# Performance work log

Measured on AMD Instinct MI355X. Metric: run time of the kernel, lower is better.

The kernel has to match this reference:

```python
import jax, jax.numpy as jnp
import numpy as np

B, S, D, H = 2, 2048, 1024, 16
HD = D // H  # 64

def setup_inputs() -> dict:
    key = jax.random.key(0)
    k1, k2, k3, k4, k5 = jax.random.split(key, 5)
    scale = 0.02
    return {
        "hidden_states": jax.random.normal(k1, (B, S, D), dtype=jnp.float32),
        "w_attn": jax.random.normal(k2, (D, 3 * D), dtype=jnp.float32) * scale,
        "b_attn": jax.random.normal(k3, (3 * D,), dtype=jnp.float32) * scale,
        "w_proj": jax.random.normal(k4, (D, D), dtype=jnp.float32) * scale,
        "b_proj": jax.random.normal(k5, (D,), dtype=jnp.float32) * scale,
    }

def reference(hidden_states, w_attn, b_attn, w_proj, b_proj):
    # qkv projection: [B,S,3D] -> split
    qkv = hidden_states @ w_attn + b_attn
    q, k, v = jnp.split(qkv, 3, axis=-1)
    # split heads -> [B,H,S,HD]
    def split_heads(t):
        return t.reshape(B, S, H, HD).transpose(0, 2, 1, 3)
    q, k, v = split_heads(q), split_heads(k), split_heads(v)
    # eager attention: full [B,H,S,S] scores, causal mask, softmax, AV
    scores = jnp.einsum('bhqd,bhkd->bhqk', q, k) / jnp.sqrt(jnp.float32(HD))
    causal = jnp.tril(jnp.ones((S, S), dtype=bool))  # [S,S]
    mask_value = jnp.finfo(scores.dtype).min
    scores = jnp.where(causal[None, None], scores, mask_value)
    attn = jax.nn.softmax(scores, axis=-1)
    out = jnp.einsum('bhqk,bhkd->bhqd', attn, v)
    # merge heads -> [B,S,D], output projection
    out = out.transpose(0, 2, 1, 3).reshape(B, S, D)
    out = out @ w_proj + b_proj
    return out
```

## Files before the change

### kernel.cpp

```cpp
#include <hip/hip_runtime.h>
#include <hip/hip_bf16.h>
#include <math.h>
#include <stdint.h>

typedef unsigned short u16;
typedef __attribute__((ext_vector_type(8))) short bf16x8;
typedef __attribute__((ext_vector_type(4))) float f32x4;

#define MFMA16(A,B,C) __builtin_amdgcn_mfma_f32_16x16x32_bf16(A,B,C,0,0,0)
#define EXP2F(x) __builtin_amdgcn_exp2f(x)

#define BB 2
#define SS 2048
#define NT (BB*SS)

__device__ __forceinline__ u16 f2bf(float f) {
    union { float f; unsigned u; } c; c.f = f;
    unsigned r = c.u + 0x7FFF + ((c.u >> 16) & 1);
    return (u16)(r >> 16);
}
__device__ __forceinline__ float bf2f(u16 v) {
    union { unsigned u; float f; } c; c.u = ((unsigned)v) << 16;
    return c.f;
}

__device__ __forceinline__ void gl_lds16(const u16* g, u16* l) {
    __builtin_amdgcn_global_load_lds(
        (const __attribute__((address_space(1))) void*)(uintptr_t)g,
        (__attribute__((address_space(3))) void*)(uintptr_t)l, 16, 0, 0);
}

__global__ __launch_bounds__(256) void cast_bf16(const float* __restrict__ in,
                                                 u16* __restrict__ out, int n) {
    int i = (blockIdx.x * 256 + threadIdx.x) * 4;
    if (i < n) {
        float4 v = *(const float4*)&in[i];
        ushort4 o;
        o.x = f2bf(v.x); o.y = f2bf(v.y); o.z = f2bf(v.z); o.w = f2bf(v.w);
        *(ushort4*)&out[i] = o;
    }
}

__global__ __launch_bounds__(256) void transpose_weights(const float* __restrict__ wa,
                                                         const float* __restrict__ wp,
                                                         u16* __restrict__ waT,
                                                         u16* __restrict__ wpT) {
    __shared__ float tile[64][65];
    const int k0 = blockIdx.x * 64;
    const bool isA = blockIdx.y < 48;
    const int m0 = (isA ? blockIdx.y : blockIdx.y - 48) * 64;
    const int M = isA ? 3072 : 1024;
    const float* in = isA ? wa : wp;
    u16* out = isA ? waT : wpT;
    const int t = threadIdx.x;
    #pragma unroll
    for (int rep = 0; rep < 16; ++rep) {
        int idx = rep * 256 + t;
        int kk = idx >> 6, mm = idx & 63;
        tile[kk][mm] = in[(size_t)(k0 + kk) * M + m0 + mm];
    }
    __syncthreads();
    #pragma unroll
    for (int rep = 0; rep < 16; ++rep) {
        int idx = rep * 256 + t;
        int mm = idx >> 6, kk = idx & 63;
        out[(size_t)(m0 + mm) * 1024 + k0 + kk] = f2bf(tile[kk][mm]);
    }
}

template<int MD, typename OutT, bool FUSE_V>
__global__ __launch_bounds__(256) void gemm_bt(const u16* __restrict__ A,
                                               const u16* __restrict__ BT,
                                               const float* __restrict__ bias,
                                               OutT* __restrict__ C,
                                               u16* __restrict__ vtg) {
    __shared__ u16 As[2][128 * 32];
    __shared__ u16 Bs[2][128 * 32];
    const int n0 = blockIdx.x * 128;
    const int m0 = blockIdx.y * 128;
    const int t = threadIdx.x;
    const int lane = t & 63;
    const int w = t >> 6;
    const int wr = (w >> 1) * 64, wc = (w & 1) * 64;
    const int ln = lane & 15, hi = lane >> 4;

    f32x4 acc[4][4];
    const f32x4 fz = {0.f, 0.f, 0.f, 0.f};
    #pragma unroll
    for (int i = 0; i < 4; ++i)
        #pragma unroll
        for (int j = 0; j < 4; ++j) acc[i][j] = fz;

    const int srow_in = lane >> 2;
    const int schunk  = lane & 3;

    #pragma unroll
    for (int p = 0; p < 2; ++p) {
        int q   = w * 2 + p;
        int row = q * 16 + srow_in;
        int cg  = schunk ^ ((row >> 1) & 3);
        gl_lds16(&A [(size_t)(n0 + row) * 1024 + cg * 8], &As[0][q * 512]);
        gl_lds16(&BT[(size_t)(m0 + row) * 1024 + cg * 8], &Bs[0][q * 512]);
    }

    for (int i = 0; i < 32; ++i) {
        const int cur = i & 1;
        __syncthreads();

        if (i < 31) {
            const int nxt = cur ^ 1;
            const int k0 = (i + 1) * 32;
            #pragma unroll
            for (int p = 0; p < 2; ++p) {
                int q   = w * 2 + p;
                int row = q * 16 + srow_in;
                int cg  = schunk ^ ((row >> 1) & 3);
                gl_lds16(&A [(size_t)(n0 + row) * 1024 + k0 + cg * 8], &As[nxt][q * 512]);
                gl_lds16(&BT[(size_t)(m0 + row) * 1024 + k0 + cg * 8], &Bs[nxt][q * 512]);
            }
        }

        bf16x8 af[4], bf[4];
        #pragma unroll
        for (int mi = 0; mi < 4; ++mi) {
            int r = wr + mi * 16 + ln;
            af[mi] = *(const bf16x8*)&As[cur][r * 32 + ((hi ^ ((r >> 1) & 3)) << 3)];
        }
        #pragma unroll
        for (int ni = 0; ni < 4; ++ni) {
            int r = wc + ni * 16 + ln;
            bf[ni] = *(const bf16x8*)&Bs[cur][r * 32 + ((hi ^ ((r >> 1) & 3)) << 3)];
        }
        __builtin_amdgcn_s_setprio(1);
        #pragma unroll
        for (int mi = 0; mi < 4; ++mi)
            #pragma unroll
            for (int ni = 0; ni < 4; ++ni)
                acc[mi][ni] = MFMA16(af[mi], bf[ni], acc[mi][ni]);
        __builtin_amdgcn_s_setprio(0);
    }

    #pragma unroll
    for (int mi = 0; mi < 4; ++mi) {
        #pragma unroll
        for (int ni = 0; ni < 4; ++ni) {
            int col = m0 + wc + ni * 16 + ln;
            float bv = bias[col];
            int row0 = n0 + wr + mi * 16 + hi * 4;
            if (FUSE_V && col >= 2048) {
                int b  = row0 >> 11;
                int s  = row0 & 2047;
                int kt = s >> 6, kl = s & 63;
                int h  = (col - 2048) >> 6, d = (col - 2048) & 63;
                int g    = (kl >> 5) * 4 + ((kl >> 2) & 3);
                int half = (kl >> 4) & 1;
                ushort4 ov;
                ov.x = f2bf(acc[mi][ni][0] + bv);
                ov.y = f2bf(acc[mi][ni][1] + bv);
                ov.z = f2bf(acc[mi][ni][2] + bv);
                ov.w = f2bf(acc[mi][ni][3] + bv);
                *(ushort4*)&vtg[(size_t)((b * 16 + h) * 32 + kt) * 4096 +
                                (size_t)(g * 64 + d) * 8 + half * 4] = ov;
            } else {
                #pragma unroll
                for (int r = 0; r < 4; ++r) {
                    float v = acc[mi][ni][r] + bv;
                    if constexpr (sizeof(OutT) == 4) C[(size_t)(row0 + r) * MD + col] = v;
                    else                             C[(size_t)(row0 + r) * MD + col] = (OutT)f2bf(v);
                }
            }
        }
    }
}

__global__ __launch_bounds__(256) void attn_mfma(const u16* __restrict__ qkv,
                                                 const u16* __restrict__ vtg,
                                                 u16* __restrict__ ctx) {
    __shared__ u16 Ks[2][64 * 64];
    __shared__ u16 Vs[2][64 * 64];
    const int bh = blockIdx.x;
    const int qt = 31 - blockIdx.y;
    const int b = bh >> 4, h = bh & 15;
    const int t = threadIdx.x, w = t >> 6, lane = t & 63;
    const int ln = lane & 15, hi = lane >> 4;
    const int qrow = qt * 64 + w * 16 + ln;
    const size_t tok = (size_t)b * SS;

    bf16x8 qb[2];
    #pragma unroll
    for (int t2 = 0; t2 < 2; ++t2) {
        bf16x8 v = *(const bf16x8*)&qkv[(tok + qrow) * 3072 + h * 64 + t2 * 32 + hi * 8];
        #pragma unroll
        for (int i = 0; i < 8; ++i)
            v[i] = (short)f2bf(bf2f((u16)v[i]) * 0.180336881f);
        qb[t2] = v;
    }

    float m_run = -1e30f, l_run = 0.f;
    f32x4 o[4];
    const f32x4 fz = {0.f, 0.f, 0.f, 0.f};
    #pragma unroll
    for (int i = 0; i < 4; ++i) o[i] = fz;

    const int kkey_l = w * 8 + (lane >> 3);
    const int ksch   = lane & 7;
    const u16* vsrc  = vtg + ((size_t)bh * 32) * 4096;

    {
        const size_t kvb = tok * 3072 + h * 64;
        #pragma unroll
        for (int p = 0; p < 2; ++p) {
            int kk = p * 32 + kkey_l;
            gl_lds16(&qkv[kvb + (size_t)kk * 3072 + 1024 + ((ksch ^ (kk & 7)) << 3)],
                     &Ks[0][(p * 32 + w * 8) * 64]);
            gl_lds16(&vsrc[(size_t)((w * 2 + p) * 64 + lane) * 8],
                     &Vs[0][(w * 2 + p) * 512]);
        }
    }

    for (int kt = 0; kt <= qt; ++kt) {
        const int cur = kt & 1;
        __syncthreads();

        if (kt < qt) {
            const int nxt = cur ^ 1;
            const size_t kvb = (tok + (kt + 1) * 64) * 3072 + h * 64;
            const u16* vs2 = vsrc + (size_t)(kt + 1) * 4096;
            #pragma unroll
            for (int p = 0; p < 2; ++p) {
                int kk = p * 32 + kkey_l;
                gl_lds16(&qkv[kvb + (size_t)kk * 3072 + 1024 + ((ksch ^ (kk & 7)) << 3)],
                         &Ks[nxt][(p * 32 + w * 8) * 64]);
                gl_lds16(&vs2[(size_t)((w * 2 + p) * 64 + lane) * 8],
                         &Vs[nxt][(w * 2 + p) * 512]);
            }
        }

        f32x4 sacc[4];
        __builtin_amdgcn_s_setprio(1);
        #pragma unroll
        for (int s = 0; s < 4; ++s) {
            int key = s * 16 + ln;
            f32x4 a = fz;
            #pragma unroll
            for (int t2 = 0; t2 < 2; ++t2) {
                bf16x8 kf = *(const bf16x8*)&Ks[cur][key * 64 + (((t2 * 4 + hi) ^ (key & 7)) << 3)];
                a = MFMA16(kf, qb[t2], a);
            }
            sacc[s] = a;
        }
        __builtin_amdgcn_s_setprio(0);

        float p_[16];
        float mloc = -1e30f;
        if (kt == qt) {
            #pragma unroll
            for (int s = 0; s < 4; ++s)
                #pragma unroll
                for (int r = 0; r < 4; ++r) {
                    int keyg = kt * 64 + s * 16 + hi * 4 + r;
                    float v = (keyg <= qrow) ? sacc[s][r] : -1e30f;
                    p_[s * 4 + r] = v;
                    mloc = fmaxf(mloc, v);
                }
        } else {
            #pragma unroll
            for (int s = 0; s < 4; ++s)
                #pragma unroll
                for (int r = 0; r < 4; ++r) {
                    float v = sacc[s][r];
                    p_[s * 4 + r] = v;
                    mloc = fmaxf(mloc, v);
                }
        }
        mloc = fmaxf(mloc, __shfl_xor(mloc, 16));
        mloc = fmaxf(mloc, __shfl_xor(mloc, 32));
        if (!__all(mloc - m_run <= 8.f)) {
            float m_new = fmaxf(m_run, mloc);
            float alpha = EXP2F(m_run - m_new);
            l_run *= alpha;
            #pragma unroll
            for (int dt = 0; dt < 4; ++dt) o[dt] *= alpha;
            m_run = m_new;
        }
        float lsum = 0.f;
        #pragma unroll
        for (int i = 0; i < 16; ++i) {
            float e = EXP2F(p_[i] - m_run);
            p_[i] = e;
            lsum += e;
        }
        lsum += __shfl_xor(lsum, 16);
        lsum += __shfl_xor(lsum, 32);
        l_run += lsum;

        bf16x8 pa[2];
        #pragma unroll
        for (int k2 = 0; k2 < 2; ++k2) {
            union { unsigned wd[4]; bf16x8 v; } pu;
            #pragma unroll
            for (int qi = 0; qi < 4; ++qi)
                asm("v_cvt_pk_bf16_f32 %0, %1, %2"
                    : "=v"(pu.wd[qi])
                    : "v"(p_[k2 * 8 + 2 * qi]), "v"(p_[k2 * 8 + 2 * qi + 1]));
            pa[k2] = pu.v;
        }

        __builtin_amdgcn_s_setprio(1);
        #pragma unroll
        for (int dt = 0; dt < 4; ++dt)
            #pragma unroll
            for (int k2 = 0; k2 < 2; ++k2) {
                bf16x8 va = *(const bf16x8*)&Vs[cur][(size_t)((k2 * 4 + hi) * 64 + dt * 16 + ln) * 8];
                o[dt] = MFMA16(va, pa[k2], o[dt]);
            }
        __builtin_amdgcn_s_setprio(0);
    }

    float inv = 1.f / l_run;
    #pragma unroll
    for (int dt = 0; dt < 4; ++dt) {
        ushort4 ov;
        ov.x = f2bf(o[dt][0] * inv);
        ov.y = f2bf(o[dt][1] * inv);
        ov.z = f2bf(o[dt][2] * inv);
        ov.w = f2bf(o[dt][3] * inv);
        *(ushort4*)&ctx[(tok + qrow) * 1024 + h * 64 + dt * 16 + hi * 4] = ov;
    }
}

extern "C" void kernel_launch(void* const* d_in, const int* in_sizes, int n_in,
                              void* d_out, int out_size, void* d_ws, size_t ws_size,
                              hipStream_t stream) {
    const float* hs     = (const float*)d_in[0];
    const float* w_attn = (const float*)d_in[1];
    const float* b_attn = (const float*)d_in[2];
    const float* w_proj = (const float*)d_in[3];
    const float* b_proj = (const float*)d_in[4];
    float* out = (float*)d_out;

    char* ws = (char*)d_ws;
    u16* hsb  = (u16*)ws;
    u16* waT  = (u16*)(ws + ((size_t)8  << 20));
    u16* wpT  = (u16*)(ws + ((size_t)14 << 20));
    u16* qkvb = (u16*)(ws + ((size_t)16 << 20));
    u16* ctxb = (u16*)(ws + ((size_t)40 << 20));
    u16* vtg  = (u16*)(ws + ((size_t)48 << 20));

    cast_bf16<<<4096, 256, 0, stream>>>(hs, hsb, NT * 1024);
    transpose_weights<<<dim3(16, 64), 256, 0, stream>>>(w_attn, w_proj, waT, wpT);

    gemm_bt<3072, u16, true><<<dim3(32, 24), 256, 0, stream>>>(hsb, waT, b_attn, qkvb, vtg);
    attn_mfma<<<dim3(BB * 16, SS / 64), 256, 0, stream>>>(qkvb, vtg, ctxb);
    gemm_bt<1024, float, false><<<dim3(32, 8), 256, 0, stream>>>(ctxb, wpT, b_proj, out, nullptr);
}
```

Measured before the change: 101.9 us.

## Pair causal query tiles per block to balance load and share K/V tiles

Each attention block now handles two query tiles, qt and 31-qt, so every block does roughly equal causal work. The K/V tiles loaded into LDS are reused by both query chains while kt <= qtA, which halves the K/V traffic for those steps and gives two independent MFMA/softmax chains to interleave. The grid shrinks from 1024 to 512 blocks, and each thread holds more registers for the second chain, which may lower occupancy.

```diff
diff --git a/kernel.cpp b/kernel.cpp
--- a/kernel.cpp
+++ b/kernel.cpp
@@ -173,34 +173,134 @@
     }
 }
 
+struct Chain {
+    float m_run, l_run;
+    f32x4 o[4];
+    bf16x8 qb[2];
+    int qrow;
+};
+
+__device__ __forceinline__ void qk_step(const u16* __restrict__ KsC,
+                                        const Chain& ch, f32x4 (&sacc)[4],
+                                        int hi, int ln) {
+    const f32x4 fz = {0.f, 0.f, 0.f, 0.f};
+    __builtin_amdgcn_s_setprio(1);
+    #pragma unroll
+    for (int s = 0; s < 4; ++s) {
+        int key = s * 16 + ln;
+        f32x4 a = fz;
+        #pragma unroll
+        for (int t2 = 0; t2 < 2; ++t2) {
+            bf16x8 kf = *(const bf16x8*)&KsC[key * 64 + (((t2 * 4 + hi) ^ (key & 7)) << 3)];
+            a = MFMA16(kf, ch.qb[t2], a);
+        }
+        sacc[s] = a;
+    }
+    __builtin_amdgcn_s_setprio(0);
+}
+
+__device__ __forceinline__ void sm_pv_step(const u16* __restrict__ VsC,
+                                           Chain& ch, f32x4 (&sacc)[4],
+                                           int kt, bool diag, int hi, int ln) {
+    float p_[16];
+    float mloc = -1e30f;
+    if (diag) {
+        #pragma unroll
+        for (int s = 0; s < 4; ++s)
+            #pragma unroll
+            for (int r = 0; r < 4; ++r) {
+                int keyg = kt * 64 + s * 16 + hi * 4 + r;
+                float v = (keyg <= ch.qrow) ? sacc[s][r] : -1e30f;
+                p_[s * 4 + r] = v;
+                mloc = fmaxf(mloc, v);
+            }
+    } else {
+        #pragma unroll
+        for (int s = 0; s < 4; ++s)
+            #pragma unroll
+            for (int r = 0; r < 4; ++r) {
+                float v = sacc[s][r];
+                p_[s * 4 + r] = v;
+                mloc = fmaxf(mloc, v);
+            }
+    }
+    mloc = fmaxf(mloc, __shfl_xor(mloc, 16));
+    mloc = fmaxf(mloc, __shfl_xor(mloc, 32));
+    if (!__all(mloc - ch.m_run <= 8.f)) {
+        float m_new = fmaxf(ch.m_run, mloc);
+        float alpha = EXP2F(ch.m_run - m_new);
+        ch.l_run *= alpha;
+        #pragma unroll
+        for (int dt = 0; dt < 4; ++dt) ch.o[dt] *= alpha;
+        ch.m_run = m_new;
+    }
+    float lsum = 0.f;
+    #pragma unroll
+    for (int i = 0; i < 16; ++i) {
+        float e = EXP2F(p_[i] - ch.m_run);
+        p_[i] = e;
+        lsum += e;
+    }
+    lsum += __shfl_xor(lsum, 16);
+    lsum += __shfl_xor(lsum, 32);
+    ch.l_run += lsum;
+
+    bf16x8 pa[2];
+    #pragma unroll
+    for (int k2 = 0; k2 < 2; ++k2) {
+        union { unsigned wd[4]; bf16x8 v; } pu;
+        #pragma unroll
+        for (int qi = 0; qi < 4; ++qi)
+            asm("v_cvt_pk_bf16_f32 %0, %1, %2"
+                : "=v"(pu.wd[qi])
+                : "v"(p_[k2 * 8 + 2 * qi]), "v"(p_[k2 * 8 + 2 * qi + 1]));
+        pa[k2] = pu.v;
+    }
+
+    __builtin_amdgcn_s_setprio(1);
+    #pragma unroll
+    for (int dt = 0; dt < 4; ++dt)
+        #pragma unroll
+        for (int k2 = 0; k2 < 2; ++k2) {
+            bf16x8 va = *(const bf16x8*)&VsC[(size_t)((k2 * 4 + hi) * 64 + dt * 16 + ln) * 8];
+            ch.o[dt] = MFMA16(va, pa[k2], ch.o[dt]);
+        }
+    __builtin_amdgcn_s_setprio(0);
+}
+
 __global__ __launch_bounds__(256) void attn_mfma(const u16* __restrict__ qkv,
                                                  const u16* __restrict__ vtg,
                                                  u16* __restrict__ ctx) {
     __shared__ u16 Ks[2][64 * 64];
     __shared__ u16 Vs[2][64 * 64];
     const int bh = blockIdx.x;
-    const int qt = 31 - blockIdx.y;
+    const int pair = blockIdx.y;
+    const int qtA = pair, qtB = 31 - pair;
     const int b = bh >> 4, h = bh & 15;
     const int t = threadIdx.x, w = t >> 6, lane = t & 63;
     const int ln = lane & 15, hi = lane >> 4;
-    const int qrow = qt * 64 + w * 16 + ln;
     const size_t tok = (size_t)b * SS;
 
-    bf16x8 qb[2];
+    const f32x4 fz = {0.f, 0.f, 0.f, 0.f};
+    Chain A, B;
+    A.qrow = qtA * 64 + w * 16 + ln;
+    B.qrow = qtB * 64 + w * 16 + ln;
+    A.m_run = B.m_run = -1e30f;
+    A.l_run = B.l_run = 0.f;
+    #pragma unroll
+    for (int i = 0; i < 4; ++i) { A.o[i] = fz; B.o[i] = fz; }
+
     #pragma unroll
     for (int t2 = 0; t2 < 2; ++t2) {
-        bf16x8 v = *(const bf16x8*)&qkv[(tok + qrow) * 3072 + h * 64 + t2 * 32 + hi * 8];
-        #pragma unroll
-        for (int i = 0; i < 8; ++i)
-            v[i] = (short)f2bf(bf2f((u16)v[i]) * 0.180336881f);
-        qb[t2] = v;
-    }
-
-    float m_run = -1e30f, l_run = 0.f;
-    f32x4 o[4];
-    const f32x4 fz = {0.f, 0.f, 0.f, 0.f};
-    #pragma unroll
-    for (int i = 0; i < 4; ++i) o[i] = fz;
+        bf16x8 va = *(const bf16x8*)&qkv[(tok + A.qrow) * 3072 + h * 64 + t2 * 32 + hi * 8];
+        bf16x8 vb = *(const bf16x8*)&qkv[(tok + B.qrow) * 3072 + h * 64 + t2 * 32 + hi * 8];
+        #pragma unroll
+        for (int i = 0; i < 8; ++i) {
+            va[i] = (short)f2bf(bf2f((u16)va[i]) * 0.180336881f);
+            vb[i] = (short)f2bf(bf2f((u16)vb[i]) * 0.180336881f);
+        }
+        A.qb[t2] = va; B.qb[t2] = vb;
+    }
 
     const int kkey_l = w * 8 + (lane >> 3);
     const int ksch   = lane & 7;
@@ -218,11 +318,11 @@
         }
     }
 
-    for (int kt = 0; kt <= qt; ++kt) {
+    for (int kt = 0; kt <= qtB; ++kt) {
         const int cur = kt & 1;
         __syncthreads();
 
-        if (kt < qt) {
+        if (kt < qtB) {
             const int nxt = cur ^ 1;
             const size_t kvb = (tok + (kt + 1) * 64) * 3072 + h * 64;
             const u16* vs2 = vsrc + (size_t)(kt + 1) * 4096;
@@ -236,96 +336,32 @@
             }
         }
 
-        f32x4 sacc[4];
-        __builtin_amdgcn_s_setprio(1);
-        #pragma unroll
-        for (int s = 0; s < 4; ++s) {
-            int key = s * 16 + ln;
-            f32x4 a = fz;
-            #pragma unroll
-            for (int t2 = 0; t2 < 2; ++t2) {
-                bf16x8 kf = *(const bf16x8*)&Ks[cur][key * 64 + (((t2 * 4 + hi) ^ (key & 7)) << 3)];
-                a = MFMA16(kf, qb[t2], a);
-            }
-            sacc[s] = a;
-        }
-        __builtin_amdgcn_s_setprio(0);
-
-        float p_[16];
-        float mloc = -1e30f;
-        if (kt == qt) {
-            #pragma unroll
-            for (int s = 0; s < 4; ++s)
-                #pragma unroll
-                for (int r = 0; r < 4; ++r) {
-                    int keyg = kt * 64 + s * 16 + hi * 4 + r;
-                    float v = (keyg <= qrow) ? sacc[s][r] : -1e30f;
-                    p_[s * 4 + r] = v;
-                    mloc = fmaxf(mloc, v);
-                }
+        const u16* KsC = &Ks[cur][0];
+        const u16* VsC = &Vs[cur][0];
+        if (kt <= qtA) {
+            f32x4 sb[4], sa[4];
+            qk_step(KsC, B, sb, hi, ln);
+            qk_step(KsC, A, sa, hi, ln);
+            sm_pv_step(VsC, B, sb, kt, false, hi, ln);
+            sm_pv_step(VsC, A, sa, kt, kt == qtA, hi, ln);
         } else {
-            #pragma unroll
-            for (int s = 0; s < 4; ++s)
-                #pragma unroll
-                for (int r = 0; r < 4; ++r) {
-                    float v = sacc[s][r];
-                    p_[s * 4 + r] = v;
-                    mloc = fmaxf(mloc, v);
-                }
-        }
-        mloc = fmaxf(mloc, __shfl_xor(mloc, 16));
-        mloc = fmaxf(mloc, __shfl_xor(mloc, 32));
-        if (!__all(mloc - m_run <= 8.f)) {
-            float m_new = fmaxf(m_run, mloc);
-            float alpha = EXP2F(m_run - m_new);
-            l_run *= alpha;
-            #pragma unroll
-            for (int dt = 0; dt < 4; ++dt) o[dt] *= alpha;
-            m_run = m_new;
-        }
-        float lsum = 0.f;
-        #pragma unroll
-        for (int i = 0; i < 16; ++i) {
-            float e = EXP2F(p_[i] - m_run);
-            p_[i] = e;
-            lsum += e;
-        }
-        lsum += __shfl_xor(lsum, 16);
-        lsum += __shfl_xor(lsum, 32);
-        l_run += lsum;
-
-        bf16x8 pa[2];
-        #pragma unroll
-        for (int k2 = 0; k2 < 2; ++k2) {
-            union { unsigned wd[4]; bf16x8 v; } pu;
-            #pragma unroll
-            for (int qi = 0; qi < 4; ++qi)
-                asm("v_cvt_pk_bf16_f32 %0, %1, %2"
-                    : "=v"(pu.wd[qi])
-                    : "v"(p_[k2 * 8 + 2 * qi]), "v"(p_[k2 * 8 + 2 * qi + 1]));
-            pa[k2] = pu.v;
-        }
-
-        __builtin_amdgcn_s_setprio(1);
-        #pragma unroll
-        for (int dt = 0; dt < 4; ++dt)
-            #pragma unroll
-            for (int k2 = 0; k2 < 2; ++k2) {
-                bf16x8 va = *(const bf16x8*)&Vs[cur][(size_t)((k2 * 4 + hi) * 64 + dt * 16 + ln) * 8];
-                o[dt] = MFMA16(va, pa[k2], o[dt]);
-            }
-        __builtin_amdgcn_s_setprio(0);
-    }
-
-    float inv = 1.f / l_run;
+            f32x4 sb[4];
+            qk_step(KsC, B, sb, hi, ln);
+            sm_pv_step(VsC, B, sb, kt, kt == qtB, hi, ln);
+        }
+    }
+
+    float invA = 1.f / A.l_run;
+    float invB = 1.f / B.l_run;
     #pragma unroll
     for (int dt = 0; dt < 4; ++dt) {
-        ushort4 ov;
-        ov.x = f2bf(o[dt][0] * inv);
-        ov.y = f2bf(o[dt][1] * inv);
-        ov.z = f2bf(o[dt][2] * inv);
-        ov.w = f2bf(o[dt][3] * inv);
-        *(ushort4*)&ctx[(tok + qrow) * 1024 + h * 64 + dt * 16 + hi * 4] = ov;
+        ushort4 oa, ob;
+        oa.x = f2bf(A.o[dt][0] * invA); oa.y = f2bf(A.o[dt][1] * invA);
+        oa.z = f2bf(A.o[dt][2] * invA); oa.w = f2bf(A.o[dt][3] * invA);
+        ob.x = f2bf(B.o[dt][0] * invB); ob.y = f2bf(B.o[dt][1] * invB);
+        ob.z = f2bf(B.o[dt][2] * invB); ob.w = f2bf(B.o[dt][3] * invB);
+        *(ushort4*)&ctx[(tok + A.qrow) * 1024 + h * 64 + dt * 16 + hi * 4] = oa;
+        *(ushort4*)&ctx[(tok + B.qrow) * 1024 + h * 64 + dt * 16 + hi * 4] = ob;
     }
 }
 
@@ -351,6 +387,6 @@
     transpose_weights<<<dim3(16, 64), 256, 0, stream>>>(w_attn, w_proj, waT, wpT);
 
     gemm_bt<3072, u16, true><<<dim3(32, 24), 256, 0, stream>>>(hsb, waT, b_attn, qkvb, vtg);
-    attn_mfma<<<dim3(BB * 16, SS / 64), 256, 0, stream>>>(qkvb, vtg, ctxb);
+    attn_mfma<<<dim3(BB * 16, 16), 256, 0, stream>>>(qkvb, vtg, ctxb);
     gemm_bt<1024, float, false><<<dim3(32, 8), 256, 0, stream>>>(ctxb, wpT, b_proj, out, nullptr);
 }
```

Result: slower. 108.0 us (+6.0%).
